# Kernel tuning notes

Measured on AMD Instinct MI355X. Metric: run time of the kernel, lower is better.

The kernel has to match this reference:

```python
import jax, jax.numpy as jnp
import numpy as np

D_MODEL = 1024
HEAD_DIM = D_MODEL // 16  # num_heads=16, used only for the softmax scale
EPS = 1e-5


def _layernorm(x, g, b):
    mu = jnp.mean(x, axis=-1, keepdims=True)
    var = jnp.var(x, axis=-1, keepdims=True)
    return (x - mu) * jax.lax.rsqrt(var + EPS) * g + b


def setup_inputs() -> dict:
    key = jax.random.key(0)
    ks = jax.random.split(key, 16)
    d, dff = D_MODEL, 4 * D_MODEL
    s = 1.0 / np.sqrt(d)
    inp = {
        "x": jax.random.normal(ks[0], (4, 2048, d), dtype=jnp.float32),
        "wq": jax.random.normal(ks[1], (d, d), dtype=jnp.float32) * s,
        "bq": jnp.zeros((d,), jnp.float32),
        "wk": jax.random.normal(ks[2], (d, d), dtype=jnp.float32) * s,
        "bk": jnp.zeros((d,), jnp.float32),
        "wv": jax.random.normal(ks[3], (d, d), dtype=jnp.float32) * s,
        "bv": jnp.zeros((d,), jnp.float32),
        "wo": jax.random.normal(ks[4], (d, d), dtype=jnp.float32) * s,
        "bo": jnp.zeros((d,), jnp.float32),
        "w1": jax.random.normal(ks[5], (d, dff), dtype=jnp.float32) * s,
        "b1": jnp.zeros((dff,), jnp.float32),
        "w2": jax.random.normal(ks[6], (dff, d), dtype=jnp.float32) * (1.0 / np.sqrt(dff)),
        "b2": jnp.zeros((d,), jnp.float32),
        "g1": jnp.ones((d,), jnp.float32),
        "be1": jnp.zeros((d,), jnp.float32),
        "g2": jnp.ones((d,), jnp.float32),
        "be2": jnp.zeros((d,), jnp.float32),
    }
    return inp


def reference(x, wq, bq, wk, bk, wv, bv, wo, bo, w1, b1, w2, b2, g1, be1, g2, be2):
    # --- attention sub-block (NOTE: no head split in original module) ---
    residual = x
    h = _layernorm(x, g1, be1)
    q = h @ wq + bq
    k = h @ wk + bk
    v = h @ wv + bv
    scale = 1.0 / np.sqrt(HEAD_DIM)
    scores = jnp.einsum("bsd,btd->bst", q, k) * scale  # [B,S,S]
    attn = jax.nn.softmax(scores, axis=-1)
    ctx = jnp.einsum("bst,btd->bsd", attn, v)
    x = ctx @ wo + bo + residual
    # --- MLP sub-block ---
    residual = x
    h = _layernorm(x, g2, be2)
    h = jax.nn.gelu(h @ w1 + b1, approximate=False)
    return h @ w2 + b2 + residual
```

## Files before the change

kernel.cpp:

```cpp
#include <hip/hip_runtime.h>
#include <hip/hip_bf16.h>

typedef __hip_bfloat16 bf16;
typedef __attribute__((ext_vector_type(8))) short short8;
typedef __attribute__((ext_vector_type(4))) float floatx4;

__device__ __forceinline__ unsigned short f2bf(float x) {
  unsigned u = __builtin_bit_cast(unsigned, x);
  unsigned r = (u + 0x7fffu + ((u >> 16) & 1u)) >> 16;
  return (unsigned short)r;
}

#define GLL(g, l) __builtin_amdgcn_global_load_lds(                                  \
    (const __attribute__((address_space(1))) void*)(g),                              \
    (__attribute__((address_space(3))) void*)(l), 16, 0, 0)

template <int N> __device__ __forceinline__ void vmwait() {
  if constexpr (N == 8) asm volatile("s_waitcnt vmcnt(8)" ::: "memory");
  else if constexpr (N == 6) asm volatile("s_waitcnt vmcnt(6)" ::: "memory");
  else if constexpr (N == 4) asm volatile("s_waitcnt vmcnt(4)" ::: "memory");
  else if constexpr (N == 3) asm volatile("s_waitcnt vmcnt(3)" ::: "memory");
  else asm volatile("s_waitcnt vmcnt(0)" ::: "memory");
}

__global__ __launch_bounds__(256) void wtrans_kernel(const float* __restrict__ in,
                                                     bf16* __restrict__ out,
                                                     int K, int N) {
  __shared__ float tile[32][33];
  int tx = threadIdx.x, ty = threadIdx.y;
  int n0 = blockIdx.x * 32, k0 = blockIdx.y * 32;
#pragma unroll
  for (int i = 0; i < 32; i += 8)
    tile[ty + i][tx] = in[(size_t)(k0 + ty + i) * N + (n0 + tx)];
  __syncthreads();
#pragma unroll
  for (int i = 0; i < 32; i += 8)
    out[(size_t)(n0 + ty + i) * K + (k0 + tx)] = __float2bfloat16(tile[tx][ty + i]);
}

__global__ __launch_bounds__(256) void btrans_kernel(const bf16* __restrict__ in,
                                                     int ldin, size_t sIn,
                                                     bf16* __restrict__ out,
                                                     int ldout, size_t sOut) {
  __shared__ bf16 tile[32][33];
  int tx = threadIdx.x, ty = threadIdx.y;
  int c0 = blockIdx.x * 32, r0 = blockIdx.y * 32;
  size_t bi = sIn * blockIdx.z, bo = sOut * blockIdx.z;
#pragma unroll
  for (int i = 0; i < 32; i += 8)
    tile[ty + i][tx] = in[bi + (size_t)(r0 + ty + i) * ldin + (c0 + tx)];
  __syncthreads();
#pragma unroll
  for (int i = 0; i < 32; i += 8)
    out[bo + (size_t)(c0 + ty + i) * ldout + (r0 + tx)] = tile[tx][ty + i];
}

__global__ __launch_bounds__(256) void ln_kernel(const float* __restrict__ x,
                                                 const float* __restrict__ g,
                                                 const float* __restrict__ b,
                                                 bf16* __restrict__ out) {
  const int D = 1024;
  size_t row = blockIdx.x;
  int t = threadIdx.x;
  float4 v = ((const float4*)(x + row * D))[t];
  float s  = v.x + v.y + v.z + v.w;
  float ss = v.x * v.x + v.y * v.y + v.z * v.z + v.w * v.w;
#pragma unroll
  for (int off = 32; off > 0; off >>= 1) {
    s  += __shfl_xor(s, off);
    ss += __shfl_xor(ss, off);
  }
  __shared__ float rs[4], rss[4];
  int wv = t >> 6;
  if ((t & 63) == 0) { rs[wv] = s; rss[wv] = ss; }
  __syncthreads();
  s  = rs[0] + rs[1] + rs[2] + rs[3];
  ss = rss[0] + rss[1] + rss[2] + rss[3];
  float mu  = s * (1.f / D);
  float inv = rsqrtf(ss * (1.f / D) - mu * mu + 1e-5f);
  float4 gv = ((const float4*)g)[t];
  float4 bv = ((const float4*)b)[t];
  ushort4 o;
  o.x = f2bf((v.x - mu) * inv * gv.x + bv.x);
  o.y = f2bf((v.y - mu) * inv * gv.y + bv.y);
  o.z = f2bf((v.z - mu) * inv * gv.z + bv.z);
  o.w = f2bf((v.w - mu) * inv * gv.w + bv.w);
  ((ushort4*)(out + row * D))[t] = o;
}

__global__ __launch_bounds__(256) void softmax_kernel(float* sc) {
  const int S = 2048;
  float* p = sc + (size_t)blockIdx.x * S;
  int t = threadIdx.x;
  float4 v0 = ((const float4*)p)[2 * t];
  float4 v1 = ((const float4*)p)[2 * t + 1];
  float f[8] = {v0.x, v0.y, v0.z, v0.w, v1.x, v1.y, v1.z, v1.w};
  float m = f[0];
#pragma unroll
  for (int j = 1; j < 8; ++j) m = fmaxf(m, f[j]);
#pragma unroll
  for (int off = 32; off > 0; off >>= 1) m = fmaxf(m, __shfl_xor(m, off));
  __shared__ float r1[4], r2[4];
  int wv = t >> 6;
  if ((t & 63) == 0) r1[wv] = m;
  __syncthreads();
  m = fmaxf(fmaxf(r1[0], r1[1]), fmaxf(r1[2], r1[3]));
  float s = 0.f;
#pragma unroll
  for (int j = 0; j < 8; ++j) { f[j] = __expf(f[j] - m); s += f[j]; }
#pragma unroll
  for (int off = 32; off > 0; off >>= 1) s += __shfl_xor(s, off);
  if ((t & 63) == 0) r2[wv] = s;
  __syncthreads();
  s = r2[0] + r2[1] + r2[2] + r2[3];
  float inv = 1.f / s;
  unsigned u0 = f2bf(f[0] * inv), u1 = f2bf(f[1] * inv);
  unsigned u2 = f2bf(f[2] * inv), u3 = f2bf(f[3] * inv);
  unsigned u4 = f2bf(f[4] * inv), u5 = f2bf(f[5] * inv);
  unsigned u6 = f2bf(f[6] * inv), u7 = f2bf(f[7] * inv);
  uint4 o;
  o.x = u0 | (u1 << 16);
  o.y = u2 | (u3 << 16);
  o.z = u4 | (u5 << 16);
  o.w = u6 | (u7 << 16);
  ((uint4*)p)[t] = o;
}

template <int NF, bool OUT_BF16, bool HAS_BIAS, bool HAS_RES, bool GELU>
__global__ __launch_bounds__(512, 2) void gemm256(
    const bf16* __restrict__ A, int lda, size_t sA,
    const bf16* __restrict__ BT, int ldb, size_t sB,
    void* Cv, size_t sC,
    const float* __restrict__ bias, const float* res,
    int N, int K, float alpha, int gx, int gy) {
  constexpr int BN = NF * 64;
  constexpr int LOADS = 2 + NF / 2;
  __shared__ bf16 As[4][256 * 32];
  __shared__ bf16 Bs[4][BN * 32];

  const int tid = threadIdx.x;
  const int lane = tid & 63;
  const int wave = tid >> 6;
  const int wm = wave >> 2, wn = wave & 3;
  const int lr = lane & 15, lq = lane >> 4;
  const int cA = (lq ^ ((lr >> 1) & 3)) * 8;

  int id = blockIdx.x;
  const int nwg = gridDim.x;
  if ((nwg & 7) == 0) id = (id & 7) * (nwg >> 3) + (id >> 3);
  const int bx = id % gx;
  const int rem = id / gx;
  const int by = rem % gy;
  const int bz = rem / gy;
  const int m0 = by * 256, n0 = bx * BN;

  const int srow = tid >> 2;
  const int kcol = ((tid & 3) ^ ((tid >> 3) & 3)) * 8;

  const bf16* ga = A + sA * bz + (size_t)(m0 + srow) * lda + kcol;
  const bf16* gb = BT + sB * bz + (size_t)(n0 + srow) * ldb + kcol;

  floatx4 acc[8][NF] = {};
  const int nk = K >> 5;

  auto stageA = [&](int u) {
    const bf16* s = ga + (size_t)u * 32;
    bf16* d = &As[u & 3][0] + tid * 8;
    GLL(s, d);
    GLL(s + (size_t)128 * lda, d + 4096);
  };
  auto stageB = [&](int u) {
    const bf16* s = gb + (size_t)u * 32;
    bf16* d = &Bs[u & 3][0] + tid * 8;
    GLL(s, d);
    if constexpr (NF == 4) GLL(s + (size_t)128 * ldb, d + 4096);
  };

  stageA(0); stageB(0);
  stageA(1); stageB(1);
  stageA(2); stageB(2);

  const int arow = wm * 128 + lr;
  const int brow = wn * (NF * 16) + lr;

  for (int t = 0; t < nk; ++t) {
    if (t + 2 < nk) vmwait<2 * LOADS>();
    else if (t + 1 < nk) vmwait<LOADS>();
    else vmwait<0>();
    __builtin_amdgcn_sched_barrier(0);
    __builtin_amdgcn_s_barrier();

    const bf16* Ab = &As[t & 3][0];
    const bf16* Bb = &Bs[t & 3][0];

    if (t + 3 < nk) stageA(t + 3);
    short8 bfrag[NF], af[4];
#pragma unroll
    for (int ni = 0; ni < NF; ++ni)
      bfrag[ni] = *(const short8*)(Bb + (brow + ni * 16) * 32 + cA);
#pragma unroll
    for (int mi = 0; mi < 4; ++mi)
      af[mi] = *(const short8*)(Ab + (arow + mi * 16) * 32 + cA);
    __builtin_amdgcn_s_setprio(1);
#pragma unroll
    for (int mi = 0; mi < 4; ++mi)
#pragma unroll
      for (int ni = 0; ni < NF; ++ni)
        acc[mi][ni] =
            __builtin_amdgcn_mfma_f32_16x16x32_bf16(af[mi], bfrag[ni], acc[mi][ni], 0, 0, 0);
    __builtin_amdgcn_s_setprio(0);
    __builtin_amdgcn_s_barrier();

    if (t + 3 < nk) stageB(t + 3);
    short8 af2[4];
#pragma unroll
    for (int mi = 0; mi < 4; ++mi)
      af2[mi] = *(const short8*)(Ab + (arow + (4 + mi) * 16) * 32 + cA);
    __builtin_amdgcn_s_setprio(1);
#pragma unroll
    for (int mi = 0; mi < 4; ++mi)
#pragma unroll
      for (int ni = 0; ni < NF; ++ni)
        acc[4 + mi][ni] =
            __builtin_amdgcn_mfma_f32_16x16x32_bf16(af2[mi], bfrag[ni], acc[4 + mi][ni], 0, 0, 0);
    __builtin_amdgcn_s_setprio(0);
    asm volatile("s_waitcnt lgkmcnt(0)" ::: "memory");
    __builtin_amdgcn_sched_barrier(0);
  }

  float* Cf = (float*)Cv;
  bf16* Cb = (bf16*)Cv;
  const size_t cb = sC * bz;
#pragma unroll
  for (int mi = 0; mi < 8; ++mi) {
    const int row = m0 + wm * 128 + mi * 16 + lq * 4;
#pragma unroll
    for (int ni = 0; ni < NF; ++ni) {
      const int col = n0 + wn * (NF * 16) + ni * 16 + lr;
      const float bb = HAS_BIAS ? bias[col] : 0.f;
#pragma unroll
      for (int r = 0; r < 4; ++r) {
        float val = acc[mi][ni][r] * alpha + bb;
        if (GELU) val = 0.5f * val * (1.f + erff(val * 0.70710678118654752f));
        if (HAS_RES) val += res[(size_t)(row + r) * N + col];
        const size_t idx = cb + (size_t)(row + r) * N + col;
        if (OUT_BF16) Cb[idx] = __float2bfloat16(val);
        else Cf[idx] = val;
      }
    }
  }
}

extern "C" void kernel_launch(void* const* d_in, const int* in_sizes, int n_in,
                              void* d_out, int out_size, void* d_ws, size_t ws_size,
                              hipStream_t stream) {
  const int B = 4, S = 2048, D = 1024, DFF = 4096;
  const int M = B * S;
  const float* x   = (const float*)d_in[0];
  const float* wq  = (const float*)d_in[1];
  const float* bq  = (const float*)d_in[2];
  const float* wk  = (const float*)d_in[3];
  const float* bk  = (const float*)d_in[4];
  const float* wv  = (const float*)d_in[5];
  const float* bv  = (const float*)d_in[6];
  const float* wo  = (const float*)d_in[7];
  const float* bo  = (const float*)d_in[8];
  const float* w1  = (const float*)d_in[9];
  const float* b1  = (const float*)d_in[10];
  const float* w2  = (const float*)d_in[11];
  const float* b2  = (const float*)d_in[12];
  const float* g1  = (const float*)d_in[13];
  const float* be1 = (const float*)d_in[14];
  const float* g2  = (const float*)d_in[15];
  const float* be2 = (const float*)d_in[16];
  float* out = (float*)d_out;

  char* wsb = (char*)d_ws;
  const size_t MB1 = 1ull << 20;
  bf16* wqkvT = (bf16*)(wsb + 0 * MB1);
  bf16* woT   = (bf16*)(wsb + 6 * MB1);
  bf16* w1T   = (bf16*)(wsb + 8 * MB1);
  bf16* w2T   = (bf16*)(wsb + 16 * MB1);
  float* bqkv = (float*)(wsb + 24 * MB1);
  bf16* h     = (bf16*)(wsb + 25 * MB1);
  bf16* qkv   = (bf16*)(wsb + 41 * MB1);
  bf16* hidden = (bf16*)(wsb + 41 * MB1);
  char* attn  = wsb + 89 * MB1;

  int chunk = 1;
  if (ws_size > 89 * MB1) {
    size_t c = (ws_size - 89 * MB1) / (20 * MB1);
    chunk = (int)(c > 4 ? 4 : (c < 1 ? 1 : c));
  }
  bf16* vTc = (bf16*)attn;
  float* sc = (float*)(attn + (size_t)chunk * 4 * MB1);

  dim3 tb(32, 8);
  wtrans_kernel<<<dim3(32, 32), tb, 0, stream>>>(wq, wqkvT, D, D);
  wtrans_kernel<<<dim3(32, 32), tb, 0, stream>>>(wk, wqkvT + (size_t)1024 * 1024, D, D);
  wtrans_kernel<<<dim3(32, 32), tb, 0, stream>>>(wv, wqkvT + (size_t)2048 * 1024, D, D);
  wtrans_kernel<<<dim3(32, 32), tb, 0, stream>>>(wo, woT, D, D);
  wtrans_kernel<<<dim3(128, 32), tb, 0, stream>>>(w1, w1T, D, DFF);
  wtrans_kernel<<<dim3(32, 128), tb, 0, stream>>>(w2, w2T, DFF, D);
  hipMemcpyAsync(bqkv, bq, 4096, hipMemcpyDeviceToDevice, stream);
  hipMemcpyAsync(bqkv + 1024, bk, 4096, hipMemcpyDeviceToDevice, stream);
  hipMemcpyAsync(bqkv + 2048, bv, 4096, hipMemcpyDeviceToDevice, stream);

  ln_kernel<<<M, 256, 0, stream>>>(x, g1, be1, h);

  gemm256<2, true, true, false, false><<<24 * 32, 512, 0, stream>>>(
      h, D, 0, wqkvT, D, 0, qkv, 0, bqkv, nullptr, 3072, D, 1.f, 24, 32);

  for (int b0 = 0; b0 < B; b0 += chunk) {
    int c = (B - b0 < chunk) ? (B - b0) : chunk;
    btrans_kernel<<<dim3(32, 64, c), tb, 0, stream>>>(
        qkv + (size_t)b0 * S * 3072 + 2048, 3072, (size_t)S * 3072,
        vTc, S, (size_t)D * S);
    gemm256<4, false, false, false, false><<<64 * c, 512, 0, stream>>>(
        qkv + (size_t)b0 * S * 3072, 3072, (size_t)S * 3072,
        qkv + (size_t)b0 * S * 3072 + 1024, 3072, (size_t)S * 3072,
        sc, (size_t)S * S, nullptr, nullptr, S, D, 0.125f, 8, 8);
    softmax_kernel<<<c * S, 256, 0, stream>>>(sc);
    gemm256<2, true, false, false, false><<<64 * c, 512, 0, stream>>>(
        (const bf16*)sc, 2 * S, (size_t)S * 2 * S,
        vTc, S, (size_t)D * S,
        h + (size_t)b0 * S * D, (size_t)S * D, nullptr, nullptr, D, S, 1.f, 8, 8);
  }

  gemm256<2, false, true, true, false><<<8 * 32, 512, 0, stream>>>(
      h, D, 0, woT, D, 0, out, 0, bo, x, D, D, 1.f, 8, 32);

  ln_kernel<<<M, 256, 0, stream>>>(out, g2, be2, h);

  gemm256<4, true, true, false, true><<<16 * 32, 512, 0, stream>>>(
      h, D, 0, w1T, D, 0, hidden, 0, b1, nullptr, DFF, D, 1.f, 16, 32);

  gemm256<2, false, true, true, false><<<8 * 32, 512, 0, stream>>>(
      hidden, DFF, 0, w2T, DFF, 0, out, 0, b2, out, D, DFF, 1.f, 8, 32);
}
```

Before: 536.2 us.

## Restructure GEMM main loop into 8-phase ping-pong pipeline with K=64 tiles

```diff
diff --git a/kernel.cpp b/kernel.cpp
--- a/kernel.cpp
+++ b/kernel.cpp
@@ -14,14 +14,6 @@
 #define GLL(g, l) __builtin_amdgcn_global_load_lds(                                  \
     (const __attribute__((address_space(1))) void*)(g),                              \
     (__attribute__((address_space(3))) void*)(l), 16, 0, 0)
-
-template <int N> __device__ __forceinline__ void vmwait() {
-  if constexpr (N == 8) asm volatile("s_waitcnt vmcnt(8)" ::: "memory");
-  else if constexpr (N == 6) asm volatile("s_waitcnt vmcnt(6)" ::: "memory");
-  else if constexpr (N == 4) asm volatile("s_waitcnt vmcnt(4)" ::: "memory");
-  else if constexpr (N == 3) asm volatile("s_waitcnt vmcnt(3)" ::: "memory");
-  else asm volatile("s_waitcnt vmcnt(0)" ::: "memory");
-}
 
 __global__ __launch_bounds__(256) void wtrans_kernel(const float* __restrict__ in,
                                                      bf16* __restrict__ out,
@@ -127,23 +119,26 @@
 }
 
 template <int NF, bool OUT_BF16, bool HAS_BIAS, bool HAS_RES, bool GELU>
-__global__ __launch_bounds__(512, 2) void gemm256(
+__global__ __launch_bounds__(512, 2) void gemm8p(
     const bf16* __restrict__ A, int lda, size_t sA,
     const bf16* __restrict__ BT, int ldb, size_t sB,
     void* Cv, size_t sC,
     const float* __restrict__ bias, const float* res,
     int N, int K, float alpha, int gx, int gy) {
   constexpr int BN = NF * 64;
-  constexpr int LOADS = 2 + NF / 2;
-  __shared__ bf16 As[4][256 * 32];
-  __shared__ bf16 Bs[4][BN * 32];
+  constexpr int LB = NF / 2;
+  constexpr int VM = 4 + 3 * LB;
+  constexpr int BSLOT = BN * 64;
+  __shared__ char lds[65536 + 4 * BSLOT + 1024];
+  char* const ldsA = lds;
+  char* const ldsB = lds + 65536;
+  char* const ldsScr = lds + 65536 + 4 * BSLOT;
 
   const int tid = threadIdx.x;
   const int lane = tid & 63;
   const int wave = tid >> 6;
   const int wm = wave >> 2, wn = wave & 3;
   const int lr = lane & 15, lq = lane >> 4;
-  const int cA = (lq ^ ((lr >> 1) & 3)) * 8;
 
   int id = blockIdx.x;
   const int nwg = gridDim.x;
@@ -154,79 +149,127 @@
   const int bz = rem / gy;
   const int m0 = by * 256, n0 = bx * BN;
 
-  const int srow = tid >> 2;
-  const int kcol = ((tid & 3) ^ ((tid >> 3) & 3)) * 8;
-
-  const bf16* ga = A + sA * bz + (size_t)(m0 + srow) * lda + kcol;
-  const bf16* gb = BT + sB * bz + (size_t)(n0 + srow) * ldb + kcol;
+  const int wrow = wave * 16 + (lane >> 2);
+  const int swzc = ((lane & 3) ^ ((lane >> 2) & 3)) * 8;
+  const bf16* gA = A + sA * bz + (size_t)(m0 + wrow) * lda + swzc;
+  const bf16* gB = BT + sB * bz + (size_t)(n0 + wrow) * ldb + swzc;
+
+  const int nk = K >> 6;
+
+  const int aBase = (wm * 128 + lr) * 64 + ((lq ^ (lr & 3)) << 4);
+  const int bBase = (wn * (NF * 16) + lr) * 64 + ((lq ^ (lr & 3)) << 4);
+
+  auto stA = [&](int tau, int h) {
+    const int tc = tau < nk ? tau : nk - 1;
+    const bf16* s = gA + (size_t)tc * 64 + h * 32;
+    if (tau < nk) {
+      char* d = ldsA + (((tau & 1) * 2 + h) << 14) + tid * 16;
+      GLL(s, d);
+      GLL(s + (size_t)128 * lda, d + 8192);
+    } else {
+      char* d = ldsScr + (lane << 4);
+      GLL(s, d);
+      GLL(s, d);
+    }
+  };
+  auto stB = [&](int tau, int h) {
+    const int tc = tau < nk ? tau : nk - 1;
+    const bf16* s = gB + (size_t)tc * 64 + h * 32;
+    if (tau < nk) {
+      char* d = ldsB + ((tau & 1) * 2 + h) * BSLOT + tid * 16;
+      GLL(s, d);
+      if constexpr (NF == 4) GLL(s + (size_t)128 * ldb, d + 8192);
+    } else {
+      char* d = ldsScr + (lane << 4);
+      GLL(s, d);
+      if constexpr (NF == 4) GLL(s, d);
+    }
+  };
 
   floatx4 acc[8][NF] = {};
-  const int nk = K >> 5;
-
-  auto stageA = [&](int u) {
-    const bf16* s = ga + (size_t)u * 32;
-    bf16* d = &As[u & 3][0] + tid * 8;
-    GLL(s, d);
-    GLL(s + (size_t)128 * lda, d + 4096);
-  };
-  auto stageB = [&](int u) {
-    const bf16* s = gb + (size_t)u * 32;
-    bf16* d = &Bs[u & 3][0] + tid * 8;
-    GLL(s, d);
-    if constexpr (NF == 4) GLL(s + (size_t)128 * ldb, d + 4096);
-  };
-
-  stageA(0); stageB(0);
-  stageA(1); stageB(1);
-  stageA(2); stageB(2);
-
-  const int arow = wm * 128 + lr;
-  const int brow = wn * (NF * 16) + lr;
+
+  stB(0, 0); stA(0, 0); stB(0, 1); stA(0, 1);
+  stB(1, 0); stA(1, 0); stB(1, 1);
+  asm volatile("s_waitcnt vmcnt(%0)" ::"i"(VM) : "memory");
+  __builtin_amdgcn_s_barrier();
 
   for (int t = 0; t < nk; ++t) {
-    if (t + 2 < nk) vmwait<2 * LOADS>();
-    else if (t + 1 < nk) vmwait<LOADS>();
-    else vmwait<0>();
-    __builtin_amdgcn_sched_barrier(0);
-    __builtin_amdgcn_s_barrier();
-
-    const bf16* Ab = &As[t & 3][0];
-    const bf16* Bb = &Bs[t & 3][0];
-
-    if (t + 3 < nk) stageA(t + 3);
-    short8 bfrag[NF], af[4];
-#pragma unroll
-    for (int ni = 0; ni < NF; ++ni)
-      bfrag[ni] = *(const short8*)(Bb + (brow + ni * 16) * 32 + cA);
-#pragma unroll
-    for (int mi = 0; mi < 4; ++mi)
-      af[mi] = *(const short8*)(Ab + (arow + mi * 16) * 32 + cA);
-    __builtin_amdgcn_s_setprio(1);
-#pragma unroll
-    for (int mi = 0; mi < 4; ++mi)
-#pragma unroll
-      for (int ni = 0; ni < NF; ++ni)
-        acc[mi][ni] =
-            __builtin_amdgcn_mfma_f32_16x16x32_bf16(af[mi], bfrag[ni], acc[mi][ni], 0, 0, 0);
-    __builtin_amdgcn_s_setprio(0);
-    __builtin_amdgcn_s_barrier();
-
-    if (t + 3 < nk) stageB(t + 3);
-    short8 af2[4];
-#pragma unroll
-    for (int mi = 0; mi < 4; ++mi)
-      af2[mi] = *(const short8*)(Ab + (arow + (4 + mi) * 16) * 32 + cA);
-    __builtin_amdgcn_s_setprio(1);
-#pragma unroll
-    for (int mi = 0; mi < 4; ++mi)
-#pragma unroll
-      for (int ni = 0; ni < NF; ++ni)
-        acc[4 + mi][ni] =
-            __builtin_amdgcn_mfma_f32_16x16x32_bf16(af2[mi], bfrag[ni], acc[4 + mi][ni], 0, 0, 0);
-    __builtin_amdgcn_s_setprio(0);
+    const char* Ak0 = ldsA + (((t & 1) * 2 + 0) << 14);
+    const char* Ak1 = ldsA + (((t & 1) * 2 + 1) << 14);
+    const char* Bk0 = ldsB + ((t & 1) * 2 + 0) * BSLOT;
+    const char* Bk1 = ldsB + ((t & 1) * 2 + 1) * BSLOT;
+
+    short8 b0[NF], a0[4];
+#pragma unroll
+    for (int ni = 0; ni < NF; ++ni) b0[ni] = *(const short8*)(Bk0 + bBase + ni * 1024);
+#pragma unroll
+    for (int mi = 0; mi < 4; ++mi) a0[mi] = *(const short8*)(Ak0 + aBase + mi * 1024);
+    stA(t + 1, 1);
+    __builtin_amdgcn_s_barrier();
     asm volatile("s_waitcnt lgkmcnt(0)" ::: "memory");
     __builtin_amdgcn_sched_barrier(0);
-  }
+    __builtin_amdgcn_s_setprio(1);
+#pragma unroll
+    for (int mi = 0; mi < 4; ++mi)
+#pragma unroll
+      for (int ni = 0; ni < NF; ++ni)
+        acc[mi][ni] = __builtin_amdgcn_mfma_f32_16x16x32_bf16(a0[mi], b0[ni], acc[mi][ni], 0, 0, 0);
+    __builtin_amdgcn_s_setprio(0);
+    __builtin_amdgcn_s_barrier();
+
+    short8 a1[4];
+#pragma unroll
+    for (int mi = 0; mi < 4; ++mi) a1[mi] = *(const short8*)(Ak0 + aBase + 4096 + mi * 1024);
+    stB(t + 2, 0);
+    __builtin_amdgcn_s_barrier();
+    asm volatile("s_waitcnt lgkmcnt(0)" ::: "memory");
+    __builtin_amdgcn_sched_barrier(0);
+    __builtin_amdgcn_s_setprio(1);
+#pragma unroll
+    for (int mi = 0; mi < 4; ++mi)
+#pragma unroll
+      for (int ni = 0; ni < NF; ++ni)
+        acc[4 + mi][ni] = __builtin_amdgcn_mfma_f32_16x16x32_bf16(a1[mi], b0[ni], acc[4 + mi][ni], 0, 0, 0);
+    __builtin_amdgcn_s_setprio(0);
+    asm volatile("s_waitcnt vmcnt(%0)" ::"i"(VM) : "memory");
+    __builtin_amdgcn_s_barrier();
+
+    short8 b1[NF], a2[4];
+#pragma unroll
+    for (int ni = 0; ni < NF; ++ni) b1[ni] = *(const short8*)(Bk1 + bBase + ni * 1024);
+#pragma unroll
+    for (int mi = 0; mi < 4; ++mi) a2[mi] = *(const short8*)(Ak1 + aBase + mi * 1024);
+    stA(t + 2, 0);
+    __builtin_amdgcn_s_barrier();
+    asm volatile("s_waitcnt lgkmcnt(0)" ::: "memory");
+    __builtin_amdgcn_sched_barrier(0);
+    __builtin_amdgcn_s_setprio(1);
+#pragma unroll
+    for (int mi = 0; mi < 4; ++mi)
+#pragma unroll
+      for (int ni = 0; ni < NF; ++ni)
+        acc[mi][ni] = __builtin_amdgcn_mfma_f32_16x16x32_bf16(a2[mi], b1[ni], acc[mi][ni], 0, 0, 0);
+    __builtin_amdgcn_s_setprio(0);
+    __builtin_amdgcn_s_barrier();
+
+    short8 a3[4];
+#pragma unroll
+    for (int mi = 0; mi < 4; ++mi) a3[mi] = *(const short8*)(Ak1 + aBase + 4096 + mi * 1024);
+    stB(t + 2, 1);
+    __builtin_amdgcn_s_barrier();
+    asm volatile("s_waitcnt lgkmcnt(0)" ::: "memory");
+    __builtin_amdgcn_sched_barrier(0);
+    __builtin_amdgcn_s_setprio(1);
+#pragma unroll
+    for (int mi = 0; mi < 4; ++mi)
+#pragma unroll
+      for (int ni = 0; ni < NF; ++ni)
+        acc[4 + mi][ni] = __builtin_amdgcn_mfma_f32_16x16x32_bf16(a3[mi], b1[ni], acc[4 + mi][ni], 0, 0, 0);
+    __builtin_amdgcn_s_setprio(0);
+    asm volatile("s_waitcnt vmcnt(%0)" ::"i"(VM) : "memory");
+    __builtin_amdgcn_s_barrier();
+  }
+  asm volatile("s_waitcnt vmcnt(0)" ::: "memory");
 
   float* Cf = (float*)Cv;
   bf16* Cb = (bf16*)Cv;
@@ -308,7 +351,7 @@
 
   ln_kernel<<<M, 256, 0, stream>>>(x, g1, be1, h);
 
-  gemm256<2, true, true, false, false><<<24 * 32, 512, 0, stream>>>(
+  gemm8p<2, true, true, false, false><<<24 * 32, 512, 0, stream>>>(
       h, D, 0, wqkvT, D, 0, qkv, 0, bqkv, nullptr, 3072, D, 1.f, 24, 32);
 
   for (int b0 = 0; b0 < B; b0 += chunk) {
@@ -316,25 +359,25 @@
     btrans_kernel<<<dim3(32, 64, c), tb, 0, stream>>>(
         qkv + (size_t)b0 * S * 3072 + 2048, 3072, (size_t)S * 3072,
         vTc, S, (size_t)D * S);
-    gemm256<4, false, false, false, false><<<64 * c, 512, 0, stream>>>(
+    gemm8p<4, false, false, false, false><<<64 * c, 512, 0, stream>>>(
         qkv + (size_t)b0 * S * 3072, 3072, (size_t)S * 3072,
         qkv + (size_t)b0 * S * 3072 + 1024, 3072, (size_t)S * 3072,
         sc, (size_t)S * S, nullptr, nullptr, S, D, 0.125f, 8, 8);
     softmax_kernel<<<c * S, 256, 0, stream>>>(sc);
-    gemm256<2, true, false, false, false><<<64 * c, 512, 0, stream>>>(
+    gemm8p<2, true, false, false, false><<<64 * c, 512, 0, stream>>>(
         (const bf16*)sc, 2 * S, (size_t)S * 2 * S,
         vTc, S, (size_t)D * S,
         h + (size_t)b0 * S * D, (size_t)S * D, nullptr, nullptr, D, S, 1.f, 8, 8);
   }
 
-  gemm256<2, false, true, true, false><<<8 * 32, 512, 0, stream>>>(
+  gemm8p<2, false, true, true, false><<<8 * 32, 512, 0, stream>>>(
       h, D, 0, woT, D, 0, out, 0, bo, x, D, D, 1.f, 8, 32);
 
   ln_kernel<<<M, 256, 0, stream>>>(out, g2, be2, h);
 
-  gemm256<4, true, true, false, true><<<16 * 32, 512, 0, stream>>>(
+  gemm8p<4, true, true, false, true><<<16 * 32, 512, 0, stream>>>(
       h, D, 0, w1T, D, 0, hidden, 0, b1, nullptr, DFF, D, 1.f, 16, 32);
 
-  gemm256<2, false, true, true, false><<<8 * 32, 512, 0, stream>>>(
+  gemm8p<2, false, true, true, false><<<8 * 32, 512, 0, stream>>>(
       hidden, DFF, 0, w2T, DFF, 0, out, 0, b2, out, D, DFF, 1.f, 8, 32);
 }
```

Result: faster. 492.0 us (-8.2%).
